# Optimization experiments

Hardware: AMD Instinct MI355X
Metric: run time of the kernel (lower is better)

The kernel has to match this reference:

```python
import jax, jax.numpy as jnp
import numpy as np

EPS = 1e-6
K = 16
TEMP = 1.0
RES_SCALE = 0.5
CLAMP_MAX = 50.0


def _knn_indices(x, k):
    # x: (B,N,3) -> idx (B,N,k), self excluded; squared dist preserves ordering
    sq = jnp.sum(x * x, axis=-1)                      # (B,N)
    d2 = sq[:, :, None] + sq[:, None, :] - 2.0 * jnp.einsum('bnd,bmd->bnm', x, x)
    N = x.shape[1]
    eye = jnp.eye(N, dtype=bool)
    d2 = jnp.where(eye[None], jnp.inf, d2)
    _, idx = jax.lax.top_k(-d2, k)
    return idx


def _gather(t, idx):
    # t: (B,N,...), idx: (B,N,k) -> (B,N,k,...)
    return jax.vmap(lambda tb, ib: tb[ib])(t, idx)


def _vn_linear(v, W):
    return jnp.einsum('bncd,oc->bnod', v, W)


def _edge_mlp(s, W1, b1, W2, b2, W3, b3):
    h = jax.nn.silu(s @ W1.T + b1)
    h = jax.nn.silu(h @ W2.T + b2)
    return h @ W3.T + b3


def _vn_layer_norm(x, gamma, beta):
    norm = jnp.maximum(jnp.linalg.norm(x, axis=-1), EPS)      # (B,N,C)
    mean = jnp.mean(norm, axis=-1, keepdims=True)
    std = jnp.maximum(jnp.std(norm, axis=-1, keepdims=True, ddof=1), EPS)
    norm_scaled = (norm - mean) / std * gamma + beta
    return x / norm[..., None] * jnp.maximum(norm_scaled[..., None], EPS)


def _clamp_features(x, max_norm):
    n = jnp.maximum(jnp.linalg.norm(x, axis=-1, keepdims=True), EPS)
    scale = jnp.minimum(max_norm / n, 1.0)
    return x * scale


def setup_inputs() -> dict:
    key = jax.random.key(0)
    ks = jax.random.split(key, 12)
    B, N, C, Cout, H = 8, 2048, 128, 128, 32
    gain = 0.5
    lim = gain * np.sqrt(6.0 / (C + Cout))
    inp = {
        'x': jax.random.normal(ks[0], (B, N, 3), jnp.float32),
        'v': jax.random.normal(ks[1], (B, N, C, 3), jnp.float32),
        'Wq': jax.random.uniform(ks[2], (Cout, C), jnp.float32, -lim, lim),
        'Wk': jax.random.uniform(ks[3], (Cout, C), jnp.float32, -lim, lim),
        'Wu': jax.random.uniform(ks[4], (Cout, C), jnp.float32, -lim, lim),
        'W1': jax.random.normal(ks[5], (H, 4), jnp.float32) * 0.3,
        'b1': jnp.zeros((H,), jnp.float32),
        'W2': jax.random.normal(ks[6], (H, H), jnp.float32) * 0.15,
        'b2': jnp.zeros((H,), jnp.float32),
        'W3': jax.random.normal(ks[7], (1, H), jnp.float32) * 0.15,
        'b3': jnp.zeros((1,), jnp.float32),
        'gamma': jnp.ones((Cout,), jnp.float32),
        'beta': jnp.zeros((Cout,), jnp.float32),
    }
    return inp


def reference(x, v, Wq, Wk, Wu, W1, b1, W2, b2, W3, b3, gamma, beta):
    idx = _knn_indices(jax.lax.stop_gradient(x), K)           # (B,N,k)
    x_nbr = _gather(x, idx)                                    # (B,N,k,3)
    Q = _vn_linear(v, Wq)                                      # (B,N,Co,3)
    Kt = _vn_linear(v, Wk)
    U = _vn_linear(v, Wu)
    K_nbr = _gather(Kt, idx)                                   # (B,N,k,Co,3)
    U_nbr = _gather(U, idx)
    qn = jnp.mean(jnp.linalg.norm(Q, axis=-1), axis=-1, keepdims=True)   # (B,N,1)
    kn = jnp.mean(jnp.linalg.norm(Kt, axis=-1), axis=-1, keepdims=True)
    kn_nbr = _gather(kn, idx)                                  # (B,N,k,1)
    dot_nbr = jnp.mean(jnp.sum(Q[:, :, None] * K_nbr, axis=-1), axis=-1, keepdims=True)  # (B,N,k,1)
    dist = jnp.linalg.norm(x[:, :, None] - x_nbr, axis=-1, keepdims=True)                # (B,N,k,1)
    qn_exp = jnp.broadcast_to(qn[:, :, None], kn_nbr.shape)
    edge_s = jnp.concatenate([qn_exp, kn_nbr, dot_nbr, dist], axis=-1)   # (B,N,k,4)
    logits = jnp.clip(_edge_mlp(edge_s, W1, b1, W2, b2, W3, b3) / TEMP, -10.0, 10.0)
    attn = jax.nn.softmax(logits, axis=2)                      # (B,N,k,1)
    msg = jnp.sum(attn[..., None] * U_nbr, axis=2)             # (B,N,Co,3)
    out = Q + RES_SCALE * msg
    out = _vn_layer_norm(out, gamma, beta)
    out = _clamp_features(out, CLAMP_MAX)
    return out
```

## Files before the change

### kernel.cpp

```cpp
#include <hip/hip_runtime.h>
#include <math.h>

#define BB 8
#define NN 2048
#define CC 128
#define KNB 16
#define BN (BB*NN)
#define WPAD 136

#define EMPTYK 0xFFFFFFFFFFFFFFFFULL

typedef __attribute__((ext_vector_type(8))) short short8;
typedef __attribute__((ext_vector_type(4))) float floatx4;
typedef __attribute__((ext_vector_type(4), aligned(4))) float floatx4u;

__device__ __forceinline__ float silu_f(float x) {
  const float e = __builtin_amdgcn_exp2f(-1.442695040888963f * x);
  return x * __builtin_amdgcn_rcpf(1.0f + e);
}
__device__ __forceinline__ float fsqrt(float x) { return __builtin_amdgcn_sqrtf(x); }
__device__ __forceinline__ float frcp(float x)  { return __builtin_amdgcn_rcpf(x); }

__device__ __forceinline__ unsigned long long umin64(unsigned long long a, unsigned long long b) {
  return (b < a) ? b : a;
}

__device__ __forceinline__ unsigned short f2bf(float f) {
  unsigned u = __float_as_uint(f);
  unsigned r = u + 0x7FFFu + ((u >> 16) & 1u);
  return (unsigned short)(r >> 16);
}
__device__ __forceinline__ float bf2f(unsigned short s) {
  return __uint_as_float(((unsigned)s) << 16);
}

__device__ __forceinline__ float dot8(const float* __restrict__ w, const float* __restrict__ h) {
  const float4 a = *(const float4*)w;
  const float4 b = *(const float4*)(w + 4);
  float s = a.x*h[0];
  s = fmaf(a.y, h[1], s); s = fmaf(a.z, h[2], s); s = fmaf(a.w, h[3], s);
  s = fmaf(b.x, h[4], s); s = fmaf(b.y, h[5], s); s = fmaf(b.z, h[6], s);
  s = fmaf(b.w, h[7], s);
  return s;
}

__global__ __launch_bounds__(256) void sq_kernel(const float* __restrict__ x,
                                                 double* __restrict__ sqd,
                                                 float4* __restrict__ x4) {
  const int i = blockIdx.x*256 + threadIdx.x;
  const float f0 = x[i*3+0], f1 = x[i*3+1], f2 = x[i*3+2];
  const double a0 = (double)f0, a1 = (double)f1, a2 = (double)f2;
  sqd[i] = a0*a0 + a1*a1 + a2*a2;
  x4[i] = make_float4(f0, f1, f2, 0.0f);
}

__global__ __launch_bounds__(256, 1) void knn_kernel(const float4* __restrict__ x4,
                                                     const double* __restrict__ sqd,
                                                     int* __restrict__ idx) {
  const int lane = threadIdx.x & 63;
  const int wave = threadIdx.x >> 6;
  const int bn = blockIdx.x * 4 + wave;
  const int b = bn >> 11;
  const int n = bn & (NN - 1);

  const float4* xb4 = x4 + (size_t)b * NN;
  const double* sqb = sqd + (size_t)b * NN;
  const float4 xq = xb4[n];
  const double xn0 = (double)xq.x, xn1 = (double)xq.y, xn2 = (double)xq.z;
  const double sqn = sqb[n];

  unsigned long long k[32];
  unsigned long long t0 = EMPTYK, t1 = EMPTYK, t2 = EMPTYK, t3 = EMPTYK;

  #pragma unroll
  for (int i = 0; i < 32; ++i) {
    const int m = i*64 + lane;
    const float4 xm = xb4[m];
    const double a0 = (double)xm.x, a1 = (double)xm.y, a2 = (double)xm.z;
    const double sqm = sqb[m];
    const double dot = xn0*a0 + xn1*a1 + xn2*a2;
    const double d = sqn + sqm - 2.0*dot;
    unsigned long long kk =
        ((unsigned long long)__double_as_longlong(d) & ~2047ULL) | (unsigned long long)m;
    if (m == n) kk = 0x8000000000000000ULL | (unsigned long long)m;
    k[i] = kk;
    const bool l3 = kk < t3, l2 = kk < t2, l1 = kk < t1, l0 = kk < t0;
    t3 = l3 ? (l2 ? t2 : kk) : t3;
    t2 = l2 ? (l1 ? t1 : kk) : t2;
    t1 = l1 ? (l0 ? t0 : kk) : t1;
    t0 = l0 ? kk : t0;
  }

  int* op = idx + (size_t)bn * KNB;
  for (int t = 0; t < KNB; ++t) {
    const unsigned h0 = (unsigned)(t0 >> 32);
    const unsigned l0w = (unsigned)t0;
    unsigned hm = h0;
    #pragma unroll
    for (int off = 32; off > 0; off >>= 1) {
      const unsigned o = (unsigned)__shfl_xor((int)hm, off, 64);
      hm = (o < hm) ? o : hm;
    }
    const bool tied = (h0 == hm);
    const unsigned long long bal = __ballot(tied);
    unsigned lm;
    if (__builtin_popcountll(bal) == 1) {
      const int owner = __builtin_ctzll(bal);
      lm = (unsigned)__shfl((int)l0w, owner, 64);
    } else {
      lm = tied ? l0w : 0xFFFFFFFFu;
      #pragma unroll
      for (int off = 32; off > 0; off >>= 1) {
        const unsigned o = (unsigned)__shfl_xor((int)lm, off, 64);
        lm = (o < lm) ? o : lm;
      }
    }
    const unsigned long long g = ((unsigned long long)hm << 32) | (unsigned long long)lm;

    if (lane == 0) op[t] = (int)(lm & 2047u);

    const bool own = tied && (l0w == lm);
    t0 = own ? t1 : t0;
    t1 = own ? t2 : t1;
    t2 = own ? t3 : t2;
    t3 = own ? EMPTYK : t3;

    const bool need = (t0 == EMPTYK);
    if (__any(need)) {
      unsigned long long nm = EMPTYK;
      #pragma unroll
      for (int i = 0; i < 32; ++i) {
        const unsigned long long c = (k[i] > g) ? k[i] : EMPTYK;
        nm = umin64(nm, c);
      }
      t0 = need ? nm : t0;
    }
  }
}

__global__ __launch_bounds__(256) void wconv_kernel(
    const float* __restrict__ Wq, const float* __restrict__ Wk, const float* __restrict__ Wu,
    unsigned short* __restrict__ Whl)
{
  const int i = blockIdx.x*256 + threadIdx.x;
  const int mat = i >> 14, rem = i & 16383;
  const float* W = (mat == 0) ? Wq : ((mat == 1) ? Wk : Wu);
  const float f = W[rem];
  const unsigned short h = f2bf(f);
  const float r = f - bf2f(h);
  unsigned short* base = Whl + (size_t)mat * 2 * CC * CC;
  base[rem]           = h;
  base[CC*CC + rem]   = f2bf(r);
}

__global__ __launch_bounds__(256, 2) void vn_gemm_mfma(
    const float* __restrict__ v, const unsigned short* __restrict__ Whl,
    float* __restrict__ Q, float* __restrict__ Kt, float* __restrict__ U)
{
  __shared__ short Wh[CC][WPAD];
  __shared__ short Wl[CC][WPAD];

  const int tid  = threadIdx.x;
  const int lane = tid & 63;
  const int wave = tid >> 6;
  const int quad = lane >> 4;
  const int l15  = lane & 15;

  const int m = blockIdx.x*64 + wave*16 + l15;
  const int p = m / 3, d = m - 3*p;
  const float* vb = v + (size_t)p * (CC*3) + d;
  float areg[32];
  #pragma unroll
  for (int kc = 0; kc < 4; ++kc)
    #pragma unroll
    for (int j = 0; j < 8; ++j)
      areg[kc*8+j] = vb[(kc*32 + quad*8 + j)*3];

  short8 ah[4], al[4];
  #pragma unroll
  for (int kc = 0; kc < 4; ++kc)
    #pragma unroll
    for (int j = 0; j < 8; ++j) {
      const float f = areg[kc*8+j];
      unsigned short h = f2bf(f);
      float r = f - bf2f(h);
      ah[kc][j] = (short)h;
      al[kc][j] = (short)f2bf(r);
    }

  const int r0s = blockIdx.x*64 + wave*16 + quad*4;
  int pbase[4];
  #pragma unroll
  for (int reg = 0; reg < 4; ++reg) {
    const int r = r0s + reg;
    const int pp = r / 3;
    pbase[reg] = pp * (CC*3) + (r - 3*pp);
  }
  const int l153 = l15 * 3;

  for (int mat = 0; mat < 3; ++mat) {
    float* __restrict__ Out = (mat == 0) ? Q : ((mat == 1) ? Kt : U);
    const unsigned short* Wg = Whl + (size_t)mat * 2 * CC * CC;

    #pragma unroll
    for (int it = 0; it < 8; ++it) {
      const int i = it*256 + tid;
      const int o = i >> 4, c8 = (i & 15) * 8;
      *(short8*)&Wh[o][c8] = *(const short8*)&Wg[o*CC + c8];
      *(short8*)&Wl[o][c8] = *(const short8*)&Wg[CC*CC + o*CC + c8];
    }
    __syncthreads();

    floatx4 acc[8];
    #pragma unroll
    for (int ct = 0; ct < 8; ++ct) acc[ct] = (floatx4){0.f, 0.f, 0.f, 0.f};

    #pragma unroll
    for (int kc = 0; kc < 4; ++kc) {
      #pragma unroll
      for (int ct = 0; ct < 8; ++ct) {
        const int o = ct*16 + l15;
        const short8 bh = *(const short8*)&Wh[o][kc*32 + quad*8];
        const short8 bl = *(const short8*)&Wl[o][kc*32 + quad*8];
        acc[ct] = __builtin_amdgcn_mfma_f32_16x16x32_bf16(ah[kc], bh, acc[ct], 0, 0, 0);
        acc[ct] = __builtin_amdgcn_mfma_f32_16x16x32_bf16(al[kc], bh, acc[ct], 0, 0, 0);
        acc[ct] = __builtin_amdgcn_mfma_f32_16x16x32_bf16(ah[kc], bl, acc[ct], 0, 0, 0);
      }
    }
    __syncthreads();

    #pragma unroll
    for (int ct = 0; ct < 8; ++ct) {
      const int o3 = ct*48 + l153;
      #pragma unroll
      for (int reg = 0; reg < 4; ++reg)
        Out[pbase[reg] + o3] = acc[ct][reg];
    }
  }
}

__global__ __launch_bounds__(256) void attn_logits_kernel(
    const float* __restrict__ x, const int* __restrict__ idx,
    const float* __restrict__ Q, const float* __restrict__ Kt,
    const float* __restrict__ W1, const float* __restrict__ b1,
    const float* __restrict__ W2, const float* __restrict__ b2,
    const float* __restrict__ W3, const float* __restrict__ b3,
    float* __restrict__ warr)
{
  const int lane = threadIdx.x & 63;
  const int wv   = threadIdx.x >> 6;
  const int bn = ((blockIdx.x & 7) << 11) | (((blockIdx.x >> 3) << 2) | wv);
  const int b = bn >> 11;

  const float* Qp = Q + (size_t)bn * (CC*3) + lane*6;
  const floatx4u q0 = *(const floatx4u*)Qp;
  const float2 q1 = *(const float2*)(Qp+4);
  const float2 qa = make_float2(q0.x, q0.y);
  const float2 qb = make_float2(q0.z, q0.w);
  const float2 qc = make_float2(q1.x, q1.y);

  const int* ip = idx + (size_t)bn * KNB;
  int j[KNB];
  #pragma unroll
  for (int t = 0; t < KNB; ++t) j[t] = ip[t];

  const int kk = lane & 15;
  int jsel = j[0];
  #pragma unroll
  for (int t = 1; t < KNB; ++t) jsel = (kk == t) ? j[t] : jsel;

  const float xi0 = x[(size_t)bn*3+0], xi1 = x[(size_t)bn*3+1], xi2 = x[(size_t)bn*3+2];
  const float* xj = x + (size_t)(b*NN + jsel)*3;
  const float xj0 = xj[0], xj1 = xj[1], xj2 = xj[2];

  float dpart[KNB], knp[KNB];
  #pragma unroll
  for (int t = 0; t < KNB; ++t) {
    const float* Kp = Kt + (size_t)(b*NN + j[t]) * (CC*3) + lane*6;
    const floatx4u kv = *(const floatx4u*)Kp;
    const float2 kw = *(const float2*)(Kp+4);
    dpart[t] = qa.x*kv.x + qa.y*kv.y + qb.x*kv.z + qb.y*kv.w + qc.x*kw.x + qc.y*kw.y;
    knp[t] = fsqrt(kv.x*kv.x + kv.y*kv.y + kv.z*kv.z) + fsqrt(kv.w*kv.w + kw.x*kw.x + kw.y*kw.y);
  }
  float qnp = fsqrt(qa.x*qa.x + qa.y*qa.y + qb.x*qb.x) + fsqrt(qb.y*qb.y + qc.x*qc.x + qc.y*qc.y);

  #pragma unroll
  for (int off = 1; off < 64; off <<= 1) qnp += __shfl_xor(qnp, off, 64);
  const float s0 = qnp * (1.0f/128.0f);

  float d8[8], k8[8];
  {
    const bool hb = (lane & 1) != 0;
    #pragma unroll
    for (int t = 0; t < 8; ++t) {
      const float dk = hb ? dpart[2*t+1] : dpart[2*t];
      const float dsn = hb ? dpart[2*t]  : dpart[2*t+1];
      const float kv = hb ? knp[2*t+1]   : knp[2*t];
      const float ksn = hb ? knp[2*t]    : knp[2*t+1];
      d8[t] = dk + __shfl_xor(dsn, 1, 64);
      k8[t] = kv + __shfl_xor(ksn, 1, 64);
    }
  }
  float d4[4], k4[4];
  {
    const bool hb = (lane & 2) != 0;
    #pragma unroll
    for (int t = 0; t < 4; ++t) {
      const float dk = hb ? d8[2*t+1] : d8[2*t];
      const float dsn = hb ? d8[2*t]  : d8[2*t+1];
      const float kv = hb ? k8[2*t+1] : k8[2*t];
      const float ksn = hb ? k8[2*t]  : k8[2*t+1];
      d4[t] = dk + __shfl_xor(dsn, 2, 64);
      k4[t] = kv + __shfl_xor(ksn, 2, 64);
    }
  }
  float d2a, d2b, k2a, k2b;
  {
    const bool hb = (lane & 4) != 0;
    const float dk0 = hb ? d4[1] : d4[0];
    const float dsn0 = hb ? d4[0] : d4[1];
    const float dk1 = hb ? d4[3] : d4[2];
    const float dsn1 = hb ? d4[2] : d4[3];
    d2a = dk0 + __shfl_xor(dsn0, 4, 64);
    d2b = dk1 + __shfl_xor(dsn1, 4, 64);
    const float kk0 = hb ? k4[1] : k4[0];
    const float ksn0 = hb ? k4[0] : k4[1];
    const float kk1 = hb ? k4[3] : k4[2];
    const float ksn1 = hb ? k4[2] : k4[3];
    k2a = kk0 + __shfl_xor(ksn0, 4, 64);
    k2b = kk1 + __shfl_xor(ksn1, 4, 64);
  }
  float dsel, knsel;
  {
    const bool hb = (lane & 8) != 0;
    const float dk = hb ? d2b : d2a;
    const float dsn = hb ? d2a : d2b;
    dsel = dk + __shfl_xor(dsn, 8, 64);
    const float kv = hb ? k2b : k2a;
    const float ksn = hb ? k2a : k2b;
    knsel = kv + __shfl_xor(ksn, 8, 64);
  }
  dsel  += __shfl_xor(dsel, 16, 64);
  dsel  += __shfl_xor(dsel, 32, 64);
  knsel += __shfl_xor(knsel, 16, 64);
  knsel += __shfl_xor(knsel, 32, 64);

  const float dx = xi0 - xj0, dy = xi1 - xj1, dz = xi2 - xj2;
  const float s3 = fsqrt(dx*dx + dy*dy + dz*dz);
  const float s1 = knsel * (1.0f/128.0f);
  const float s2 = dsel * (1.0f/128.0f);

  const int g = lane >> 4;
  const int o0 = g*8, o1 = (g^1)*8, o2 = (g^2)*8, o3 = (g^3)*8;

  float h1o[8];
  {
    const float4 b1a = *(const float4*)(b1 + o0);
    const float4 b1b = *(const float4*)(b1 + o0 + 4);
    const float bb1[8] = {b1a.x,b1a.y,b1a.z,b1a.w,b1b.x,b1b.y,b1b.z,b1b.w};
    #pragma unroll
    for (int jj = 0; jj < 8; ++jj) {
      const float4 w = *(const float4*)(W1 + (o0 + jj)*4);
      float u = bb1[jj];
      u = fmaf(w.x, s0, u); u = fmaf(w.y, s1, u);
      u = fmaf(w.z, s2, u); u = fmaf(w.w, s3, u);
      h1o[jj] = silu_f(u);
    }
  }
  float hx16[8], hx32[8], hx48[8];
  #pragma unroll
  for (int jj = 0; jj < 8; ++jj) hx16[jj] = __shfl_xor(h1o[jj], 16, 64);
  #pragma unroll
  for (int jj = 0; jj < 8; ++jj) hx32[jj] = __shfl_xor(h1o[jj], 32, 64);
  #pragma unroll
  for (int jj = 0; jj < 8; ++jj) hx48[jj] = __shfl_xor(hx16[jj], 32, 64);

  float logit;
  {
    const float4 b2a = *(const float4*)(b2 + o0);
    const float4 b2b = *(const float4*)(b2 + o0 + 4);
    const float bb2[8] = {b2a.x,b2a.y,b2a.z,b2a.w,b2b.x,b2b.y,b2b.z,b2b.w};
    const float4 w3a = *(const float4*)(W3 + o0);
    const float4 w3b = *(const float4*)(W3 + o0 + 4);
    const float ww3[8] = {w3a.x,w3a.y,w3a.z,w3a.w,w3b.x,w3b.y,w3b.z,w3b.w};
    float lp = 0.f;
    #pragma unroll
    for (int hh = 0; hh < 8; ++hh) {
      const float* wr = W2 + (o0 + hh)*32;
      float a = bb2[hh];
      a += dot8(wr + o0, h1o);
      a += dot8(wr + o1, hx16);
      a += dot8(wr + o2, hx32);
      a += dot8(wr + o3, hx48);
      lp = fmaf(ww3[hh], silu_f(a), lp);
    }
    lp += __shfl_xor(lp, 16, 64);
    lp += __shfl_xor(lp, 32, 64);
    logit = lp + b3[0];
  }
  logit = fminf(fmaxf(logit, -10.0f), 10.0f);

  float mx = logit;
  #pragma unroll
  for (int off = 8; off > 0; off >>= 1) mx = fmaxf(mx, __shfl_xor(mx, off, 16));
  const float e = __builtin_amdgcn_exp2f(1.442695040888963f * (logit - mx));
  float ssum = e;
  #pragma unroll
  for (int off = 8; off > 0; off >>= 1) ssum += __shfl_xor(ssum, off, 16);
  const float w = e * frcp(ssum);

  if (lane < KNB) warr[(size_t)bn * KNB + lane] = w;
}

__global__ __launch_bounds__(256) void attn_msg_kernel(
    const int* __restrict__ idx, const float* __restrict__ Q,
    const float* __restrict__ U, const float* __restrict__ warr,
    const float* __restrict__ gam, const float* __restrict__ bet,
    float* __restrict__ out)
{
  const int lane = threadIdx.x & 63;
  const int wv   = threadIdx.x >> 6;
  const int bn = ((blockIdx.x & 7) << 11) | (((blockIdx.x >> 3) << 2) | wv);
  const int b = bn >> 11;

  const int* ip = idx + (size_t)bn * KNB;
  int j[KNB];
  #pragma unroll
  for (int t = 0; t < KNB; ++t) j[t] = ip[t];

  const float* Qp = Q + (size_t)bn * (CC*3) + lane*6;
  const floatx4u q0 = *(const floatx4u*)Qp;
  const float2 q1 = *(const float2*)(Qp+4);

  const float* wp = warr + (size_t)bn * KNB;
  float wk[KNB];
  #pragma unroll
  for (int t = 0; t < KNB; ++t) wk[t] = wp[t];

  float m0=0.f,m1=0.f,m2=0.f,m3=0.f,m4=0.f,m5=0.f;
  #pragma unroll
  for (int t = 0; t < KNB; ++t) {
    const float* Up = U + (size_t)(b*NN + j[t]) * (CC*3) + lane*6;
    const floatx4u uv = *(const floatx4u*)Up;
    const float2 uw = *(const float2*)(Up+4);
    const float ww = wk[t];
    m0 = fmaf(ww, uv.x, m0); m1 = fmaf(ww, uv.y, m1); m2 = fmaf(ww, uv.z, m2);
    m3 = fmaf(ww, uv.w, m3); m4 = fmaf(ww, uw.x, m4); m5 = fmaf(ww, uw.y, m5);
  }
  const float oa0 = q0.x + 0.5f*m0, oa1 = q0.y + 0.5f*m1, oa2 = q0.z + 0.5f*m2;
  const float ob0 = q0.w + 0.5f*m3, ob1 = q1.x + 0.5f*m4, ob2 = q1.y + 0.5f*m5;

  const float na = fmaxf(fsqrt(oa0*oa0 + oa1*oa1 + oa2*oa2), 1e-6f);
  const float nb = fmaxf(fsqrt(ob0*ob0 + ob1*ob1 + ob2*ob2), 1e-6f);
  float s = na + nb;
  #pragma unroll
  for (int off = 1; off < 64; off <<= 1) s += __shfl_xor(s, off, 64);
  const float mean = s * (1.0f/128.0f);
  const float dva = na - mean, dvb = nb - mean;
  float s2v = dva*dva + dvb*dvb;
  #pragma unroll
  for (int off = 1; off < 64; off <<= 1) s2v += __shfl_xor(s2v, off, 64);
  const float stdv = fmaxf(fsqrt(s2v * (1.0f/127.0f)), 1e-6f);
  const float rstd = frcp(stdv);

  const float2 gm = *(const float2*)(gam + lane*2);
  const float2 bt = *(const float2*)(bet + lane*2);
  const float nsa = (na - mean) * rstd * gm.x + bt.x;
  const float nsb = (nb - mean) * rstd * gm.y + bt.y;
  const float sca = fmaxf(nsa, 1e-6f) * frcp(na);
  const float scb = fmaxf(nsb, 1e-6f) * frcp(nb);
  float fa0 = oa0*sca, fa1 = oa1*sca, fa2 = oa2*sca;
  float fb0 = ob0*scb, fb1 = ob1*scb, fb2 = ob2*scb;
  const float n2a = fmaxf(fsqrt(fa0*fa0 + fa1*fa1 + fa2*fa2), 1e-6f);
  const float n2b = fmaxf(fsqrt(fb0*fb0 + fb1*fb1 + fb2*fb2), 1e-6f);
  const float c2a = fminf(50.0f * frcp(n2a), 1.0f);
  const float c2b = fminf(50.0f * frcp(n2b), 1.0f);

  float* op = out + (size_t)bn * (CC*3) + lane*6;
  floatx4u o4; o4.x = fa0*c2a; o4.y = fa1*c2a; o4.z = fa2*c2a; o4.w = fb0*c2b;
  *(floatx4u*)op = o4;
  *(float2*)(op+4) = make_float2(fb1*c2b, fb2*c2b);
}

extern "C" void kernel_launch(void* const* d_in, const int* in_sizes, int n_in,
                              void* d_out, int out_size, void* d_ws, size_t ws_size,
                              hipStream_t stream) {
  (void)in_sizes; (void)n_in; (void)out_size; (void)ws_size;
  const float* x   = (const float*)d_in[0];
  const float* v   = (const float*)d_in[1];
  const float* Wq  = (const float*)d_in[2];
  const float* Wk  = (const float*)d_in[3];
  const float* Wu  = (const float*)d_in[4];
  const float* W1  = (const float*)d_in[5];
  const float* b1  = (const float*)d_in[6];
  const float* W2  = (const float*)d_in[7];
  const float* b2  = (const float*)d_in[8];
  const float* W3  = (const float*)d_in[9];
  const float* b3  = (const float*)d_in[10];
  const float* gam = (const float*)d_in[11];
  const float* bet = (const float*)d_in[12];
  float* out = (float*)d_out;

  char* ws = (char*)d_ws;
  int*   idx = (int*)ws;
  float* Q   = (float*)(ws + (size_t)BN * KNB * 4);
  float* Kt  = Q  + (size_t)BN * CC * 3;
  float* U   = Kt + (size_t)BN * CC * 3;
  unsigned short* Whl = (unsigned short*)(U + (size_t)BN * CC * 3);
  float* warr = (float*)((char*)Whl + (size_t)3 * 2 * CC * CC * 2);
  double* sqd = (double*)(warr + (size_t)BN * KNB);
  float4* x4  = (float4*)(sqd + (size_t)BN);

  sq_kernel<<<BN/256, 256, 0, stream>>>(x, sqd, x4);
  knn_kernel<<<BN/4, 256, 0, stream>>>(x4, sqd, idx);
  wconv_kernel<<<192, 256, 0, stream>>>(Wq, Wk, Wu, Whl);
  vn_gemm_mfma<<<(BN*3)/64, 256, 0, stream>>>(v, Whl, Q, Kt, U);
  attn_logits_kernel<<<BN/4, 256, 0, stream>>>(x, idx, Q, Kt,
                                               W1, b1, W2, b2, W3, b3, warr);
  attn_msg_kernel<<<BN/4, 256, 0, stream>>>(idx, Q, U, warr, gam, bet, out);
}
```

Before: 277.7 us.

## Recompute kNN distances instead of caching, stage edge-MLP weights in LDS

The kNN kernel no longer keeps all 32 candidate keys in registers. Instead it recomputes distances during the rare refill scans, and the launch bound drops its min-blocks hint and the unroll is reduced. This is meant to lower register pressure and raise occupancy, at the cost of extra global loads and recomputation whenever a lane's top-4 list runs dry. Separately, the attention-logit kernel loads the MLP weights and biases into shared memory once per block, replacing the per-lane global reads in the MLP. That adds a block-wide barrier.

```diff
diff --git a/kernel.cpp b/kernel.cpp
--- a/kernel.cpp
+++ b/kernel.cpp
@@ -54,9 +54,9 @@
   x4[i] = make_float4(f0, f1, f2, 0.0f);
 }
 
-__global__ __launch_bounds__(256, 1) void knn_kernel(const float4* __restrict__ x4,
-                                                     const double* __restrict__ sqd,
-                                                     int* __restrict__ idx) {
+__global__ __launch_bounds__(256) void knn_kernel(const float4* __restrict__ x4,
+                                                  const double* __restrict__ sqd,
+                                                  int* __restrict__ idx) {
   const int lane = threadIdx.x & 63;
   const int wave = threadIdx.x >> 6;
   const int bn = blockIdx.x * 4 + wave;
@@ -69,10 +69,9 @@
   const double xn0 = (double)xq.x, xn1 = (double)xq.y, xn2 = (double)xq.z;
   const double sqn = sqb[n];
 
-  unsigned long long k[32];
   unsigned long long t0 = EMPTYK, t1 = EMPTYK, t2 = EMPTYK, t3 = EMPTYK;
 
-  #pragma unroll
+  #pragma unroll 8
   for (int i = 0; i < 32; ++i) {
     const int m = i*64 + lane;
     const float4 xm = xb4[m];
@@ -83,7 +82,6 @@
     unsigned long long kk =
         ((unsigned long long)__double_as_longlong(d) & ~2047ULL) | (unsigned long long)m;
     if (m == n) kk = 0x8000000000000000ULL | (unsigned long long)m;
-    k[i] = kk;
     const bool l3 = kk < t3, l2 = kk < t2, l1 = kk < t1, l0 = kk < t0;
     t3 = l3 ? (l2 ? t2 : kk) : t3;
     t2 = l2 ? (l1 ? t1 : kk) : t2;
@@ -128,9 +126,18 @@
     const bool need = (t0 == EMPTYK);
     if (__any(need)) {
       unsigned long long nm = EMPTYK;
-      #pragma unroll
+      #pragma unroll 1
       for (int i = 0; i < 32; ++i) {
-        const unsigned long long c = (k[i] > g) ? k[i] : EMPTYK;
+        const int m = i*64 + lane;
+        const float4 xm = xb4[m];
+        const double a0 = (double)xm.x, a1 = (double)xm.y, a2 = (double)xm.z;
+        const double sqm = sqb[m];
+        const double dot = xn0*a0 + xn1*a1 + xn2*a2;
+        const double d = sqn + sqm - 2.0*dot;
+        unsigned long long kk =
+            ((unsigned long long)__double_as_longlong(d) & ~2047ULL) | (unsigned long long)m;
+        if (m == n) kk = 0x8000000000000000ULL | (unsigned long long)m;
+        const unsigned long long c = (kk > g) ? kk : EMPTYK;
         nm = umin64(nm, c);
       }
       t0 = need ? nm : t0;
@@ -247,22 +254,39 @@
     const float* __restrict__ W3, const float* __restrict__ b3,
     float* __restrict__ warr)
 {
-  const int lane = threadIdx.x & 63;
-  const int wv   = threadIdx.x >> 6;
+  __shared__ __align__(16) float W2s[32][32];
+  __shared__ __align__(16) float W1s[32][4];
+  __shared__ __align__(16) float b1s[32];
+  __shared__ __align__(16) float b2s[32];
+  __shared__ __align__(16) float W3s[32];
+  __shared__ float b3s;
+
+  const int tid  = threadIdx.x;
+  const int lane = tid & 63;
+  const int wv   = tid >> 6;
   const int bn = ((blockIdx.x & 7) << 11) | (((blockIdx.x >> 3) << 2) | wv);
   const int b = bn >> 11;
 
   const float* Qp = Q + (size_t)bn * (CC*3) + lane*6;
   const floatx4u q0 = *(const floatx4u*)Qp;
   const float2 q1 = *(const float2*)(Qp+4);
+
+  const int* ip = idx + (size_t)bn * KNB;
+  int j[KNB];
+  #pragma unroll
+  for (int t = 0; t < KNB; ++t) j[t] = ip[t];
+
+  #pragma unroll
+  for (int it = 0; it < 4; ++it)
+    ((float*)W2s)[it*256 + tid] = W2[it*256 + tid];
+  if (tid < 128) ((float*)W1s)[tid] = W1[tid];
+  if (tid < 32) { b1s[tid] = b1[tid]; b2s[tid] = b2[tid]; W3s[tid] = W3[tid]; }
+  if (tid == 0) b3s = b3[0];
+  __syncthreads();
+
   const float2 qa = make_float2(q0.x, q0.y);
   const float2 qb = make_float2(q0.z, q0.w);
   const float2 qc = make_float2(q1.x, q1.y);
-
-  const int* ip = idx + (size_t)bn * KNB;
-  int j[KNB];
-  #pragma unroll
-  for (int t = 0; t < KNB; ++t) j[t] = ip[t];
 
   const int kk = lane & 15;
   int jsel = j[0];
@@ -355,12 +379,12 @@
 
   float h1o[8];
   {
-    const float4 b1a = *(const float4*)(b1 + o0);
-    const float4 b1b = *(const float4*)(b1 + o0 + 4);
+    const float4 b1a = *(const float4*)&b1s[o0];
+    const float4 b1b = *(const float4*)&b1s[o0 + 4];
     const float bb1[8] = {b1a.x,b1a.y,b1a.z,b1a.w,b1b.x,b1b.y,b1b.z,b1b.w};
     #pragma unroll
     for (int jj = 0; jj < 8; ++jj) {
-      const float4 w = *(const float4*)(W1 + (o0 + jj)*4);
+      const float4 w = *(const float4*)&W1s[o0 + jj][0];
       float u = bb1[jj];
       u = fmaf(w.x, s0, u); u = fmaf(w.y, s1, u);
       u = fmaf(w.z, s2, u); u = fmaf(w.w, s3, u);
@@ -377,16 +401,16 @@
 
   float logit;
   {
-    const float4 b2a = *(const float4*)(b2 + o0);
-    const float4 b2b = *(const float4*)(b2 + o0 + 4);
+    const float4 b2a = *(const float4*)&b2s[o0];
+    const float4 b2b = *(const float4*)&b2s[o0 + 4];
     const float bb2[8] = {b2a.x,b2a.y,b2a.z,b2a.w,b2b.x,b2b.y,b2b.z,b2b.w};
-    const float4 w3a = *(const float4*)(W3 + o0);
-    const float4 w3b = *(const float4*)(W3 + o0 + 4);
+    const float4 w3a = *(const float4*)&W3s[o0];
+    const float4 w3b = *(const float4*)&W3s[o0 + 4];
     const float ww3[8] = {w3a.x,w3a.y,w3a.z,w3a.w,w3b.x,w3b.y,w3b.z,w3b.w};
     float lp = 0.f;
     #pragma unroll
     for (int hh = 0; hh < 8; ++hh) {
-      const float* wr = W2 + (o0 + hh)*32;
+      const float* wr = &W2s[o0 + hh][0];
       float a = bb2[hh];
       a += dot8(wr + o0, h1o);
       a += dot8(wr + o1, hx16);
@@ -396,7 +420,7 @@
     }
     lp += __shfl_xor(lp, 16, 64);
     lp += __shfl_xor(lp, 32, 64);
-    logit = lp + b3[0];
+    logit = lp + b3s;
   }
   logit = fminf(fmaxf(logit, -10.0f), 10.0f);
 
```

Result: faster. 252.4 us (-9.1%).
